# Kernel tuning notes

Measured on AMD Instinct MI355X. Metric: run time of the kernel, lower is better.

Reference implementation:

```python
import jax, jax.numpy as jnp
import numpy as np

B, L, D, H = 2, 2048, 1024, 16
DH = D // H  # per-head dim = 64


def setup_inputs() -> dict:
    key = jax.random.key(0)
    ks = jax.random.split(key, 7)
    s = 1.0 / np.sqrt(D)
    x = jax.random.normal(ks[0], (B, L, D), dtype=jnp.float32)
    Wq = jax.random.normal(ks[1], (D, D), dtype=jnp.float32) * s
    bq = jax.random.normal(ks[2], (D,), dtype=jnp.float32) * s
    Wk = jax.random.normal(ks[3], (D, D), dtype=jnp.float32) * s
    bk = jax.random.normal(ks[4], (D,), dtype=jnp.float32) * s
    Wv = jax.random.normal(ks[5], (D, D), dtype=jnp.float32) * s
    bv = jax.random.normal(ks[6], (D,), dtype=jnp.float32) * s
    # strict upper-triangular causal mask; mask==1 means position is masked (-inf)
    atten_mask = jnp.triu(jnp.ones((L, L), dtype=jnp.int32), k=1)
    return {"x": x, "atten_mask": atten_mask, "Wq": Wq, "bq": bq,
            "Wk": Wk, "bk": bk, "Wv": Wv, "bv": bv}


def reference(x, atten_mask, Wq, bq, Wk, bk, Wv, bv):
    # nn.Linear: y = x @ W^T + b
    q = x @ Wq.T + bq  # [B,L,D]
    k = x @ Wk.T + bk
    v = x @ Wv.T + bv
    # contiguous split into heads == reshape to [B,L,H,DH]
    q = q.reshape(B, L, H, DH)
    k = k.reshape(B, L, H, DH)
    v = v.reshape(B, L, H, DH)
    scale = jnp.sqrt(jnp.float32(DH))
    scores = jnp.einsum('blhd,bmhd->bhlm', q, k) / scale  # [B,H,L,L]
    # torch.where(mask == 1, -inf, scores)
    scores = jnp.where(atten_mask[None, None] == 1, -jnp.inf, scores)
    attn = jax.nn.softmax(scores, axis=-1)
    out = jnp.einsum('bhlm,bmhd->blhd', attn, v)  # [B,L,H,DH]
    return out.reshape(B, L, D)  # concat heads along channel dim
```

## Files before the change

### kernel.cpp

```cpp
#include <hip/hip_runtime.h>
#include <hip/hip_bf16.h>

#define BDIM 2
#define LSEQ 2048
#define DMODEL 1024
#define NH 16
#define DHEAD 64
#define SP 72
#define CTS 136

typedef __bf16 bf16_t;
typedef __attribute__((ext_vector_type(8))) __bf16 bf16x8;
typedef __attribute__((ext_vector_type(4))) __bf16 bf16x4;
typedef __attribute__((ext_vector_type(2))) __bf16 bf16x2;
typedef __attribute__((ext_vector_type(4))) float f32x4;
typedef __attribute__((ext_vector_type(4))) int i32x4;

static __device__ __forceinline__ f32x4 mfma16(bf16x8 a, bf16x8 b, f32x4 c) {
    return __builtin_amdgcn_mfma_f32_16x16x32_bf16(a, b, c, 0, 0, 0);
}

static __device__ __forceinline__ void load_lds16(const bf16_t* g, void* l) {
    __builtin_amdgcn_global_load_lds(
        (const __attribute__((address_space(1))) void*)g,
        (__attribute__((address_space(3))) void*)l, 16, 0, 0);
}

__global__ void convert_all(
    const float* __restrict__ x,
    const float* __restrict__ Wq, const float* __restrict__ Wk, const float* __restrict__ Wv,
    const float* __restrict__ bq, const float* __restrict__ bk, const float* __restrict__ bv,
    bf16_t* __restrict__ cx,
    bf16_t* __restrict__ cWq, bf16_t* __restrict__ cWk, bf16_t* __restrict__ cWv,
    bf16_t* __restrict__ cbq, bf16_t* __restrict__ cbk, bf16_t* __restrict__ cbv,
    float SQ)
{
    const int blk = blockIdx.x;
    const float* src; bf16_t* dst; int base, cnt; float sc = 1.0f;
    if (blk < 1024)      { src = x;  dst = cx;  base = blk * 1024;          cnt = 1024; }
    else if (blk < 1280) { src = Wq; dst = cWq; base = (blk - 1024) * 1024; cnt = 1024; sc = SQ; }
    else if (blk < 1536) { src = Wk; dst = cWk; base = (blk - 1280) * 1024; cnt = 1024; }
    else if (blk < 1792) { src = Wv; dst = cWv; base = (blk - 1536) * 1024; cnt = 1024; }
    else if (blk == 1792){ src = bq; dst = cbq; base = 0; cnt = 256; sc = SQ; }
    else if (blk == 1793){ src = bk; dst = cbk; base = 0; cnt = 256; }
    else                 { src = bv; dst = cbv; base = 0; cnt = 256; }

    for (int i = base + threadIdx.x; i < base + cnt; i += 256) {
        f32x4 v = *(const f32x4*)(src + 4 * (size_t)i);
        bf16x4 o;
        o[0] = (bf16_t)(v[0] * sc); o[1] = (bf16_t)(v[1] * sc);
        o[2] = (bf16_t)(v[2] * sc); o[3] = (bf16_t)(v[3] * sc);
        *(bf16x4*)(dst + 4 * (size_t)i) = o;
    }
}

__global__ __launch_bounds__(512, 2) void qkv_gemm(
    const bf16_t* __restrict__ x,
    const bf16_t* __restrict__ W0, const bf16_t* __restrict__ W1, const bf16_t* __restrict__ W2,
    const bf16_t* __restrict__ b0, const bf16_t* __restrict__ b1, const bf16_t* __restrict__ b2,
    bf16_t* __restrict__ yq, bf16_t* __restrict__ yk, bf16_t* __restrict__ yvT)
{
    __shared__ alignas(16) bf16_t smem[65536];

    const int tid  = threadIdx.x;
    const int lane = tid & 63;
    const int w    = tid >> 6;
    const int quad = lane >> 4;
    const int n16  = lane & 15;
    const int swz  = n16 & 7;
    const int srow = lane >> 3;
    const int schnk = (lane & 7) ^ srow;

    const int s   = blockIdx.x;
    const int sem = ((s & 7) << 3) | (s >> 3);
    const int m0  = (sem >> 2) * 256;
    const int n0  = (sem & 3) * 256;
    const int z   = blockIdx.y;

    const bf16_t* W    = (z == 0) ? W0 : ((z == 1) ? W1 : W2);
    const bf16_t* bias = (z == 0) ? b0 : ((z == 1) ? b1 : b2);

    const int wm = (w >> 2) * 128;
    const int wn = (w & 3) * 64;

    const bf16_t* gA = x + (size_t)(m0 + w * 8 + srow) * DMODEL + schnk * 8;
    const bf16_t* gB = W + (size_t)(n0 + w * 8 + srow) * DMODEL + schnk * 8;

    f32x4 acc[8][4] = {};

    auto stageA = [&](int buf, int h, int kt) {
        bf16_t* d = smem + buf * 32768 + (h * 128 + w * 8) * 64;
        const bf16_t* src = gA + (size_t)(h * 128) * DMODEL + kt * 64;
        load_lds16(src, d);
        load_lds16(src + (size_t)64 * DMODEL, d + 64 * 64);
    };
    auto stageB = [&](int buf, int h, int kt) {
        bf16_t* d = smem + buf * 32768 + 16384 + (h * 128 + w * 8) * 64;
        const bf16_t* src = gB + (size_t)(h * 128) * DMODEL + kt * 64;
        load_lds16(src, d);
        load_lds16(src + (size_t)64 * DMODEL, d + 64 * 64);
    };

    stageA(0, 0, 0); stageA(0, 1, 0);
    stageB(0, 0, 0); stageB(0, 1, 0);
    stageB(1, 0, 1); stageB(1, 1, 1);
    asm volatile("s_waitcnt vmcnt(4)" ::: "memory");
    __builtin_amdgcn_s_barrier();

    for (int u = 0; u < 16; ++u) {
        const int buf = u & 1;
        const bf16_t* Ab = smem + buf * 32768;
        const bf16_t* Bb = Ab + 16384;

        bf16x8 bfr[4][2], aX[2][2], aY[2][2];

        #pragma unroll
        for (int nt = 0; nt < 4; ++nt) {
            const bf16_t* br = Bb + (wn + nt * 16 + n16) * 64;
            bfr[nt][0] = *(const bf16x8*)(br + ((quad    ) ^ swz) * 8);
            bfr[nt][1] = *(const bf16x8*)(br + ((quad + 4) ^ swz) * 8);
        }
        #pragma unroll
        for (int m2 = 0; m2 < 2; ++m2) {
            const bf16_t* ar = Ab + (wm + m2 * 16 + n16) * 64;
            aX[m2][0] = *(const bf16x8*)(ar + ((quad    ) ^ swz) * 8);
            aX[m2][1] = *(const bf16x8*)(ar + ((quad + 4) ^ swz) * 8);
        }
        if (u + 1 < 16) { stageA(buf ^ 1, 0, u + 1); stageA(buf ^ 1, 1, u + 1); }
        asm volatile("s_waitcnt lgkmcnt(0)" ::: "memory");
        __builtin_amdgcn_s_barrier();
        if (u + 2 < 16) stageB(buf, 0, u + 2);

        #pragma unroll
        for (int m2 = 0; m2 < 2; ++m2) {
            const bf16_t* ar = Ab + (wm + (2 + m2) * 16 + n16) * 64;
            aY[m2][0] = *(const bf16x8*)(ar + ((quad    ) ^ swz) * 8);
            aY[m2][1] = *(const bf16x8*)(ar + ((quad + 4) ^ swz) * 8);
        }
        #pragma unroll
        for (int m2 = 0; m2 < 2; ++m2)
            #pragma unroll
            for (int nt = 0; nt < 4; ++nt) {
                acc[m2][nt] = mfma16(aX[m2][0], bfr[nt][0], acc[m2][nt]);
                acc[m2][nt] = mfma16(aX[m2][1], bfr[nt][1], acc[m2][nt]);
            }
        if (u + 2 < 16) stageB(buf, 1, u + 2);

        #pragma unroll
        for (int m2 = 0; m2 < 2; ++m2) {
            const bf16_t* ar = Ab + (wm + (4 + m2) * 16 + n16) * 64;
            aX[m2][0] = *(const bf16x8*)(ar + ((quad    ) ^ swz) * 8);
            aX[m2][1] = *(const bf16x8*)(ar + ((quad + 4) ^ swz) * 8);
        }
        #pragma unroll
        for (int m2 = 0; m2 < 2; ++m2)
            #pragma unroll
            for (int nt = 0; nt < 4; ++nt) {
                acc[2 + m2][nt] = mfma16(aY[m2][0], bfr[nt][0], acc[2 + m2][nt]);
                acc[2 + m2][nt] = mfma16(aY[m2][1], bfr[nt][1], acc[2 + m2][nt]);
            }

        #pragma unroll
        for (int m2 = 0; m2 < 2; ++m2) {
            const bf16_t* ar = Ab + (wm + (6 + m2) * 16 + n16) * 64;
            aY[m2][0] = *(const bf16x8*)(ar + ((quad    ) ^ swz) * 8);
            aY[m2][1] = *(const bf16x8*)(ar + ((quad + 4) ^ swz) * 8);
        }
        #pragma unroll
        for (int m2 = 0; m2 < 2; ++m2)
            #pragma unroll
            for (int nt = 0; nt < 4; ++nt) {
                acc[4 + m2][nt] = mfma16(aX[m2][0], bfr[nt][0], acc[4 + m2][nt]);
                acc[4 + m2][nt] = mfma16(aX[m2][1], bfr[nt][1], acc[4 + m2][nt]);
            }

        #pragma unroll
        for (int m2 = 0; m2 < 2; ++m2)
            #pragma unroll
            for (int nt = 0; nt < 4; ++nt) {
                acc[6 + m2][nt] = mfma16(aY[m2][0], bfr[nt][0], acc[6 + m2][nt]);
                acc[6 + m2][nt] = mfma16(aY[m2][1], bfr[nt][1], acc[6 + m2][nt]);
            }

        if (u < 14) asm volatile("s_waitcnt vmcnt(4)" ::: "memory");
        else        asm volatile("s_waitcnt vmcnt(0)" ::: "memory");
        __builtin_amdgcn_s_barrier();
    }

    if (z < 2) {
        bf16_t* y = (z == 0) ? yq : yk;
        bf16_t* Ct = smem;
        #pragma unroll
        for (int hp = 0; hp < 2; ++hp) {
            if (((w & 3) >> 1) == hp) {
                #pragma unroll
                for (int nt = 0; nt < 4; ++nt) {
                    const int jc = (w & 1) * 64 + nt * 16 + n16;
                    const float bv = (float)bias[n0 + hp * 128 + jc];
                    #pragma unroll
                    for (int mt = 0; mt < 8; ++mt) {
                        const int rr = wm + mt * 16 + quad * 4;
                        #pragma unroll
                        for (int r = 0; r < 4; ++r)
                            Ct[(rr + r) * CTS + jc] = (bf16_t)(acc[mt][nt][r] + bv);
                    }
                }
            }
            __syncthreads();
            const int row = tid >> 1;
            const int seg = tid & 1;
            const int hh  = (n0 >> 6) + hp * 2 + seg;
            const int i   = m0 + row;
            const int bb  = i >> 11, ll = i & 2047;
            bf16_t* dst = &y[(((size_t)bb * NH + hh) * LSEQ + ll) * DHEAD];
            const bf16_t* srcr = &Ct[row * CTS + seg * 64];
            #pragma unroll
            for (int c = 0; c < 8; ++c)
                *(bf16x8*)(dst + c * 8) = *(const bf16x8*)(srcr + c * 8);
            __syncthreads();
        }
    } else {
        #pragma unroll
        for (int nt = 0; nt < 4; ++nt) {
            const int j = n0 + wn + nt * 16 + n16;
            const float bv = (float)bias[j];
            #pragma unroll
            for (int mt = 0; mt < 8; ++mt) {
                const int i0 = m0 + wm + mt * 16 + quad * 4;
                const int bb = i0 >> 11, l = i0 & 2047;
                bf16x4 pk;
                #pragma unroll
                for (int r = 0; r < 4; ++r) pk[r] = (bf16_t)(acc[mt][nt][r] + bv);
                *(bf16x4*)(&yvT[((size_t)bb * DMODEL + j) * LSEQ + l]) = pk;
            }
        }
    }
}

__global__ __launch_bounds__(256) void attn_fused(
    const bf16_t* __restrict__ qp,
    const bf16_t* __restrict__ kp,
    const bf16_t* __restrict__ vtp,
    float* __restrict__ out,
    float* __restrict__ Opart,
    float* __restrict__ ml)
{
    __shared__ alignas(16) bf16_t Ks[2][64 * 64];
    __shared__ alignas(16) bf16_t Vs[2][64 * 64];
    __shared__ alignas(16) bf16_t Pw[4][2][32 * SP];

    const int tid  = threadIdx.x;
    const int lane = tid & 63;
    const int w    = tid >> 6;
    const int quad = lane >> 4;
    const int n16  = lane & 15;
    const int lane3 = lane >> 3;
    const int lane7 = lane & 7;
    const int swz8  = (lane7 ^ lane3) * 8;
    const int swz   = n16 & 7;

    const int bh  = blockIdx.x;
    const int yy  = blockIdx.y;
    const int p   = yy & 7;
    const bool isA = (yy < 8);
    const int b = bh >> 4, h = bh & 15;
    const size_t hb = (size_t)bh * (LSEQ * DHEAD);

    float l_[2];
    f32x4 oacc[2][4];

    auto process = [&](int qt, int t0, int ntiles, bool maskTail) {
        int iqg[2];
        bf16x8 qb[2][2];
        #pragma unroll
        for (int g = 0; g < 2; ++g) {
            iqg[g] = qt * 128 + 32 * w + 16 * g + n16;
            const bf16_t* qq = qp + hb + (size_t)iqg[g] * DHEAD;
            qb[g][0] = *(const bf16x8*)(qq + quad * 8);
            qb[g][1] = *(const bf16x8*)(qq + 32 + quad * 8);
        }

        const bf16_t* gk = kp  + hb + (size_t)(t0 * 64 + 16 * w + lane3) * DHEAD + swz8;
        const bf16_t* gv = vtp + hb + (size_t)(16 * w + lane3) * LSEQ + t0 * 64 + swz8;

        int buf = 0;
        {
            char* lk = (char*)&Ks[0][0] + w * 2048;
            char* lv = (char*)&Vs[0][0] + w * 2048;
            load_lds16(gk,             lk);
            load_lds16(gk + 8 * DHEAD, lk + 1024);
            load_lds16(gv,             lv);
            load_lds16(gv + 8 * LSEQ,  lv + 1024);
            gk += 64 * DHEAD; gv += 64;
        }
        __syncthreads();

        for (int it = 0; it < ntiles; ++it) {
            if (it + 1 < ntiles) {
                char* lk = (char*)&Ks[buf ^ 1][0] + w * 2048;
                char* lv = (char*)&Vs[buf ^ 1][0] + w * 2048;
                load_lds16(gk,             lk);
                load_lds16(gk + 8 * DHEAD, lk + 1024);
                load_lds16(gv,             lv);
                load_lds16(gv + 8 * LSEQ,  lv + 1024);
                gk += 64 * DHEAD; gv += 64;
            }

            const bf16_t* kb = &Ks[buf][0];
            f32x4 s[2][4];
            #pragma unroll
            for (int t = 0; t < 4; ++t) {
                const bf16_t* krow = kb + (t * 16 + n16) * 64;
                bf16x8 k0v = *(const bf16x8*)(krow + ((quad    ) ^ swz) * 8);
                bf16x8 k1v = *(const bf16x8*)(krow + ((quad + 4) ^ swz) * 8);
                #pragma unroll
                for (int g = 0; g < 2; ++g) {
                    f32x4 z = {0.f, 0.f, 0.f, 0.f};
                    z = mfma16(k0v, qb[g][0], z);
                    z = mfma16(k1v, qb[g][1], z);
                    s[g][t] = z;
                }
            }

            if (maskTail && it >= ntiles - 2) {
                const int k0 = (t0 + it) * 64;
                #pragma unroll
                for (int g = 0; g < 2; ++g)
                    #pragma unroll
                    for (int t = 0; t < 4; ++t)
                        #pragma unroll
                        for (int r = 0; r < 4; ++r)
                            if (k0 + t * 16 + quad * 4 + r > iqg[g]) s[g][t][r] = -1e30f;
            }

            #pragma unroll
            for (int g = 0; g < 2; ++g) {
                bf16_t* pw = &Pw[w][buf][g * 16 * SP] + n16 * SP + quad * 4;
                float rs = 0.f;
                #pragma unroll
                for (int t = 0; t < 4; ++t) {
                    float p0 = __builtin_amdgcn_exp2f(s[g][t][0]);
                    float p1 = __builtin_amdgcn_exp2f(s[g][t][1]);
                    float p2 = __builtin_amdgcn_exp2f(s[g][t][2]);
                    float p3 = __builtin_amdgcn_exp2f(s[g][t][3]);
                    rs += (p0 + p1) + (p2 + p3);
                    bf16x4 pk;
                    pk[0] = (bf16_t)p0; pk[1] = (bf16_t)p1;
                    pk[2] = (bf16_t)p2; pk[3] = (bf16_t)p3;
                    *(bf16x4*)(pw + t * 16) = pk;
                }
                l_[g] += rs;
            }

            asm volatile("s_waitcnt lgkmcnt(0)" ::: "memory");

            const bf16_t* vbs = &Vs[buf][0];
            #pragma unroll
            for (int c = 0; c < 2; ++c) {
                bf16x8 pb0 = *(const bf16x8*)(&Pw[w][buf][0]       + n16 * SP + c * 32 + quad * 8);
                bf16x8 pb1 = *(const bf16x8*)(&Pw[w][buf][16 * SP] + n16 * SP + c * 32 + quad * 8);
                #pragma unroll
                for (int t = 0; t < 4; ++t) {
                    const bf16_t* vrow = vbs + (t * 16 + n16) * 64;
                    bf16x8 va = *(const bf16x8*)(vrow + ((quad + 4 * c) ^ swz) * 8);
                    oacc[0][t] = mfma16(va, pb0, oacc[0][t]);
                    oacc[1][t] = mfma16(va, pb1, oacc[1][t]);
                }
            }

            __syncthreads();
            buf ^= 1;
        }
    };

    auto zero_state = [&]() {
        #pragma unroll
        for (int g = 0; g < 2; ++g) {
            l_[g] = 0.f;
            #pragma unroll
            for (int t = 0; t < 4; ++t) { f32x4 zz = {0.f,0.f,0.f,0.f}; oacc[g][t] = zz; }
        }
    };

    auto store_partial = [&](int pidx) {
        #pragma unroll
        for (int g = 0; g < 2; ++g) {
            float ls = l_[g];
            ls += __shfl_xor(ls, 16, 64);
            ls += __shfl_xor(ls, 32, 64);
            const int row = 32 * w + 16 * g + n16;
            float* Ob = Opart + (size_t)pidx * (128 * 64) + row * 64;
            #pragma unroll
            for (int t = 0; t < 4; ++t)
                *(f32x4*)(Ob + t * 16 + quad * 4) = oacc[g][t];
            if (quad == 0) ml[(size_t)pidx * 128 + row] = ls;
        }
    };

    if (isA) {
        zero_state();
        process(p, 0, 2 * p + 2, true);
        #pragma unroll
        for (int g = 0; g < 2; ++g) {
            float ls = l_[g];
            ls += __shfl_xor(ls, 16, 64);
            ls += __shfl_xor(ls, 32, 64);
            const float inv = 1.0f / ls;
            const int iq = p * 128 + 32 * w + 16 * g + n16;
            float* orow = out + ((size_t)b * LSEQ + iq) * DMODEL + h * DHEAD;
            #pragma unroll
            for (int t = 0; t < 4; ++t) {
                f32x4 o;
                o[0] = oacc[g][t][0] * inv; o[1] = oacc[g][t][1] * inv;
                o[2] = oacc[g][t][2] * inv; o[3] = oacc[g][t][3] * inv;
                *(f32x4*)(orow + t * 16 + quad * 4) = o;
            }
        }
        zero_state();
        process(15 - p, 0, 15 - 2 * p, false);
        store_partial((bh * 8 + (7 - p)) * 2 + 0);
    } else {
        zero_state();
        process(15 - p, 15 - 2 * p, 17, true);
        store_partial((bh * 8 + (7 - p)) * 2 + 1);
    }
}

__global__ __launch_bounds__(256) void attn_combine(
    const float* __restrict__ Opart, const float* __restrict__ ml,
    float* __restrict__ out)
{
    const int bh = blockIdx.x;
    const int q8 = blockIdx.y;
    const int t  = threadIdx.x;
    const int row = t >> 1;
    const int dh0 = (t & 1) * 32;
    const int p0  = (bh * 8 + q8) * 2;
    const int b = bh >> 4, h = bh & 15;

    float l0 = ml[(size_t)p0 * 128 + row];
    float l1 = ml[(size_t)(p0 + 1) * 128 + row];
    float inv = 1.0f / (l0 + l1);

    const float* P0 = Opart + (size_t)p0 * (128 * 64) + row * 64 + dh0;
    const float* P1 = P0 + 128 * 64;
    float* orow = out + ((size_t)b * LSEQ + ((8 + q8) * 128 + row)) * DMODEL
                + h * DHEAD + dh0;
    #pragma unroll
    for (int c = 0; c < 8; ++c) {
        f32x4 o0 = *(const f32x4*)(P0 + 4 * c);
        f32x4 o1 = *(const f32x4*)(P1 + 4 * c);
        f32x4 o;
        o[0] = (o0[0] + o1[0]) * inv;
        o[1] = (o0[1] + o1[1]) * inv;
        o[2] = (o0[2] + o1[2]) * inv;
        o[3] = (o0[3] + o1[3]) * inv;
        *(f32x4*)(orow + 4 * c) = o;
    }
}

extern "C" void kernel_launch(void* const* d_in, const int* in_sizes, int n_in,
                              void* d_out, int out_size, void* d_ws, size_t ws_size,
                              hipStream_t stream)
{
    const float* x  = (const float*)d_in[0];
    const float* Wq = (const float*)d_in[2];
    const float* bq = (const float*)d_in[3];
    const float* Wk = (const float*)d_in[4];
    const float* bk = (const float*)d_in[5];
    const float* Wv = (const float*)d_in[6];
    const float* bv = (const float*)d_in[7];
    float* out = (float*)d_out;

    char* ws = (char*)d_ws;
    bf16_t* q   = (bf16_t*)(ws);
    bf16_t* k   = (bf16_t*)(ws + 8u  * 1024 * 1024);
    bf16_t* vT  = (bf16_t*)(ws + 16u * 1024 * 1024);
    bf16_t* cx  = (bf16_t*)(ws + 24u * 1024 * 1024);
    bf16_t* cWq = (bf16_t*)(ws + 32u * 1024 * 1024);
    bf16_t* cWk = (bf16_t*)(ws + 34u * 1024 * 1024);
    bf16_t* cWv = (bf16_t*)(ws + 36u * 1024 * 1024);
    bf16_t* cbq = (bf16_t*)(ws + 38u * 1024 * 1024);
    bf16_t* cbk = (bf16_t*)(ws + 38u * 1024 * 1024 + 4096);
    bf16_t* cbv = (bf16_t*)(ws + 38u * 1024 * 1024 + 8192);
    float*  mlp = (float*) (ws + 39u * 1024 * 1024);
    float*  Op  = (float*) (ws + 40u * 1024 * 1024);

    const float SQ = 0.125f * 1.44269504088896f;

    convert_all<<<1795, 256, 0, stream>>>(x, Wq, Wk, Wv, bq, bk, bv,
                                          cx, cWq, cWk, cWv, cbq, cbk, cbv, SQ);

    dim3 g1(64, 3, 1);
    qkv_gemm<<<g1, 512, 0, stream>>>(cx, cWq, cWk, cWv, cbq, cbk, cbv, q, k, vT);

    dim3 g2(BDIM * NH, 16, 1);
    attn_fused<<<g2, 256, 0, stream>>>(q, k, vT, out, Op, mlp);

    dim3 g3(BDIM * NH, 8, 1);
    attn_combine<<<g3, 256, 0, stream>>>(Op, mlp, out);
}
```

Before: 171.1 us.

## Load V tiles straight into registers with double buffering instead of LDS

Drops the shared-memory V buffers in the fused attention kernel. Each wave now loads its V operand fragments directly from global memory into a pair of register arrays, prefetching the next tile while the current one is used, and the loop is unrolled by two to alternate buffers. A min-blocks hint of 2 is added to launch bounds, aiming for higher occupancy now that LDS use is smaller. In exchange, every wave reads the whole V tile on its own, so global/L2 traffic for V grows fourfold with short 64-byte row segments, and the extra register arrays raise VGPR pressure.

Result: slower. 179.2 us (+4.7%).

```diff
diff --git a/kernel.cpp b/kernel.cpp
--- a/kernel.cpp
+++ b/kernel.cpp
@@ -237,7 +237,7 @@
     }
 }
 
-__global__ __launch_bounds__(256) void attn_fused(
+__global__ __launch_bounds__(256, 2) void attn_fused(
     const bf16_t* __restrict__ qp,
     const bf16_t* __restrict__ kp,
     const bf16_t* __restrict__ vtp,
@@ -246,7 +246,6 @@
     float* __restrict__ ml)
 {
     __shared__ alignas(16) bf16_t Ks[2][64 * 64];
-    __shared__ alignas(16) bf16_t Vs[2][64 * 64];
     __shared__ alignas(16) bf16_t Pw[4][2][32 * SP];
 
     const int tid  = threadIdx.x;
@@ -280,30 +279,36 @@
             qb[g][1] = *(const bf16x8*)(qq + 32 + quad * 8);
         }
 
-        const bf16_t* gk = kp  + hb + (size_t)(t0 * 64 + 16 * w + lane3) * DHEAD + swz8;
-        const bf16_t* gv = vtp + hb + (size_t)(16 * w + lane3) * LSEQ + t0 * 64 + swz8;
+        const bf16_t* gk = kp + hb + (size_t)(t0 * 64 + 16 * w + lane3) * DHEAD + swz8;
+        const bf16_t* gvl = vtp + hb + (size_t)n16 * LSEQ + (size_t)t0 * 64 + quad * 8;
+
+        bf16x8 vA[8], vB[8];
+        auto loadV = [&](bf16x8 (&vv)[8], int it) {
+            const bf16_t* pv = gvl + it * 64;
+            #pragma unroll
+            for (int c = 0; c < 2; ++c)
+                #pragma unroll
+                for (int t = 0; t < 4; ++t)
+                    vv[c * 4 + t] = *(const bf16x8*)(pv + (size_t)(t * 16) * LSEQ + c * 32);
+        };
 
         int buf = 0;
         {
             char* lk = (char*)&Ks[0][0] + w * 2048;
-            char* lv = (char*)&Vs[0][0] + w * 2048;
             load_lds16(gk,             lk);
             load_lds16(gk + 8 * DHEAD, lk + 1024);
-            load_lds16(gv,             lv);
-            load_lds16(gv + 8 * LSEQ,  lv + 1024);
-            gk += 64 * DHEAD; gv += 64;
-        }
+            gk += 64 * DHEAD;
+        }
+        loadV(vA, 0);
         __syncthreads();
 
-        for (int it = 0; it < ntiles; ++it) {
+        auto body = [&](int it, bf16x8 (&vcur)[8], bf16x8 (&vnext)[8]) {
             if (it + 1 < ntiles) {
                 char* lk = (char*)&Ks[buf ^ 1][0] + w * 2048;
-                char* lv = (char*)&Vs[buf ^ 1][0] + w * 2048;
                 load_lds16(gk,             lk);
                 load_lds16(gk + 8 * DHEAD, lk + 1024);
-                load_lds16(gv,             lv);
-                load_lds16(gv + 8 * LSEQ,  lv + 1024);
-                gk += 64 * DHEAD; gv += 64;
+                gk += 64 * DHEAD;
+                loadV(vnext, it + 1);
             }
 
             const bf16_t* kb = &Ks[buf][0];
@@ -354,15 +359,13 @@
 
             asm volatile("s_waitcnt lgkmcnt(0)" ::: "memory");
 
-            const bf16_t* vbs = &Vs[buf][0];
             #pragma unroll
             for (int c = 0; c < 2; ++c) {
                 bf16x8 pb0 = *(const bf16x8*)(&Pw[w][buf][0]       + n16 * SP + c * 32 + quad * 8);
                 bf16x8 pb1 = *(const bf16x8*)(&Pw[w][buf][16 * SP] + n16 * SP + c * 32 + quad * 8);
                 #pragma unroll
                 for (int t = 0; t < 4; ++t) {
-                    const bf16_t* vrow = vbs + (t * 16 + n16) * 64;
-                    bf16x8 va = *(const bf16x8*)(vrow + ((quad + 4 * c) ^ swz) * 8);
+                    bf16x8 va = vcur[c * 4 + t];
                     oacc[0][t] = mfma16(va, pb0, oacc[0][t]);
                     oacc[1][t] = mfma16(va, pb1, oacc[1][t]);
                 }
@@ -370,7 +373,14 @@
 
             __syncthreads();
             buf ^= 1;
-        }
+        };
+
+        int it = 0;
+        for (; it + 2 <= ntiles; it += 2) {
+            body(it,     vA, vB);
+            body(it + 1, vB, vA);
+        }
+        if (it < ntiles) body(it, vA, vB);
     };
 
     auto zero_state = [&]() {
```

## Split attention waves 2x2 over query rows and key halves with LDS pair reduction

Applied to the files above, without the earlier changes.

Each pair of waves now covers 64 query rows, and each wave in the pair handles half of the 64 keys in every tile. This doubles reuse of each K/V LDS fragment per MFMA, and the two partial outputs and row sums are reduced through shared memory at the end. The LDS layout becomes a single 72KB arena that is shared with the reduction buffer, and launch bounds request two blocks per CU. The costs are higher register pressure (16 accumulator tiles per wave), a larger LDS footprint, and extra synchronisation in the reduction. Odd waves also sit idle during the epilogue.

Result: faster. 167.2 us (-2.3%).

```diff
diff --git a/kernel.cpp b/kernel.cpp
--- a/kernel.cpp
+++ b/kernel.cpp
@@ -6,7 +6,8 @@
 #define DMODEL 1024
 #define NH 16
 #define DHEAD 64
-#define SP 72
+#define SP 40
+#define RST 68
 #define CTS 136
 
 typedef __bf16 bf16_t;
@@ -237,7 +238,7 @@
     }
 }
 
-__global__ __launch_bounds__(256) void attn_fused(
+__global__ __launch_bounds__(256, 2) void attn_fused(
     const bf16_t* __restrict__ qp,
     const bf16_t* __restrict__ kp,
     const bf16_t* __restrict__ vtp,
@@ -245,9 +246,11 @@
     float* __restrict__ Opart,
     float* __restrict__ ml)
 {
-    __shared__ alignas(16) bf16_t Ks[2][64 * 64];
-    __shared__ alignas(16) bf16_t Vs[2][64 * 64];
-    __shared__ alignas(16) bf16_t Pw[4][2][32 * SP];
+    __shared__ alignas(16) char arena[73728];
+    bf16_t* KsB = (bf16_t*)(arena);
+    bf16_t* VsB = (bf16_t*)(arena + 16384);
+    bf16_t* PwB = (bf16_t*)(arena + 32768);
+    float*  Rex = (float*) (arena + 32768);
 
     const int tid  = threadIdx.x;
     const int lane = tid & 63;
@@ -259,6 +262,12 @@
     const int swz8  = (lane7 ^ lane3) * 8;
     const int swz   = n16 & 7;
 
+    const int wq   = (w >> 1) * 64;
+    const int wkv  = (w & 1) * 32;
+    const int pairI = w >> 1;
+    const bool isOdd = (w & 1) != 0;
+    bf16_t* Pw0 = PwB + w * (2 * 64 * SP);
+
     const int bh  = blockIdx.x;
     const int yy  = blockIdx.y;
     const int p   = yy & 7;
@@ -266,15 +275,24 @@
     const int b = bh >> 4, h = bh & 15;
     const size_t hb = (size_t)bh * (LSEQ * DHEAD);
 
-    float l_[2];
-    f32x4 oacc[2][4];
+    float l_[4];
+    f32x4 oacc[4][4];
+
+    auto zero_state = [&]() {
+        #pragma unroll
+        for (int g = 0; g < 4; ++g) {
+            l_[g] = 0.f;
+            #pragma unroll
+            for (int mv = 0; mv < 4; ++mv) { f32x4 zz = {0.f,0.f,0.f,0.f}; oacc[mv][g] = zz; }
+        }
+    };
 
     auto process = [&](int qt, int t0, int ntiles, bool maskTail) {
-        int iqg[2];
-        bf16x8 qb[2][2];
-        #pragma unroll
-        for (int g = 0; g < 2; ++g) {
-            iqg[g] = qt * 128 + 32 * w + 16 * g + n16;
+        int iqg[4];
+        bf16x8 qb[4][2];
+        #pragma unroll
+        for (int g = 0; g < 4; ++g) {
+            iqg[g] = qt * 128 + wq + 16 * g + n16;
             const bf16_t* qq = qp + hb + (size_t)iqg[g] * DHEAD;
             qb[g][0] = *(const bf16x8*)(qq + quad * 8);
             qb[g][1] = *(const bf16x8*)(qq + 32 + quad * 8);
@@ -285,8 +303,8 @@
 
         int buf = 0;
         {
-            char* lk = (char*)&Ks[0][0] + w * 2048;
-            char* lv = (char*)&Vs[0][0] + w * 2048;
+            char* lk = (char*)KsB + w * 2048;
+            char* lv = (char*)VsB + w * 2048;
             load_lds16(gk,             lk);
             load_lds16(gk + 8 * DHEAD, lk + 1024);
             load_lds16(gv,             lv);
@@ -297,8 +315,8 @@
 
         for (int it = 0; it < ntiles; ++it) {
             if (it + 1 < ntiles) {
-                char* lk = (char*)&Ks[buf ^ 1][0] + w * 2048;
-                char* lv = (char*)&Vs[buf ^ 1][0] + w * 2048;
+                char* lk = (char*)KsB + (buf ^ 1) * 8192 + w * 2048;
+                char* lv = (char*)VsB + (buf ^ 1) * 8192 + w * 2048;
                 load_lds16(gk,             lk);
                 load_lds16(gk + 8 * DHEAD, lk + 1024);
                 load_lds16(gv,             lv);
@@ -306,66 +324,66 @@
                 gk += 64 * DHEAD; gv += 64;
             }
 
-            const bf16_t* kb = &Ks[buf][0];
+            const bf16_t* kb = KsB + buf * 4096;
             f32x4 s[2][4];
             #pragma unroll
-            for (int t = 0; t < 4; ++t) {
-                const bf16_t* krow = kb + (t * 16 + n16) * 64;
+            for (int m = 0; m < 2; ++m) {
+                const bf16_t* krow = kb + (wkv + 16 * m + n16) * 64;
                 bf16x8 k0v = *(const bf16x8*)(krow + ((quad    ) ^ swz) * 8);
                 bf16x8 k1v = *(const bf16x8*)(krow + ((quad + 4) ^ swz) * 8);
                 #pragma unroll
-                for (int g = 0; g < 2; ++g) {
+                for (int g = 0; g < 4; ++g) {
                     f32x4 z = {0.f, 0.f, 0.f, 0.f};
                     z = mfma16(k0v, qb[g][0], z);
                     z = mfma16(k1v, qb[g][1], z);
-                    s[g][t] = z;
+                    s[m][g] = z;
                 }
             }
 
             if (maskTail && it >= ntiles - 2) {
-                const int k0 = (t0 + it) * 64;
-                #pragma unroll
-                for (int g = 0; g < 2; ++g)
+                const int k0 = (t0 + it) * 64 + wkv;
+                #pragma unroll
+                for (int m = 0; m < 2; ++m)
                     #pragma unroll
-                    for (int t = 0; t < 4; ++t)
+                    for (int g = 0; g < 4; ++g)
                         #pragma unroll
                         for (int r = 0; r < 4; ++r)
-                            if (k0 + t * 16 + quad * 4 + r > iqg[g]) s[g][t][r] = -1e30f;
-            }
-
-            #pragma unroll
-            for (int g = 0; g < 2; ++g) {
-                bf16_t* pw = &Pw[w][buf][g * 16 * SP] + n16 * SP + quad * 4;
+                            if (k0 + 16 * m + quad * 4 + r > iqg[g]) s[m][g][r] = -1e30f;
+            }
+
+            bf16_t* pwb = Pw0 + buf * (64 * SP);
+            #pragma unroll
+            for (int g = 0; g < 4; ++g) {
                 float rs = 0.f;
                 #pragma unroll
-                for (int t = 0; t < 4; ++t) {
-                    float p0 = __builtin_amdgcn_exp2f(s[g][t][0]);
-                    float p1 = __builtin_amdgcn_exp2f(s[g][t][1]);
-                    float p2 = __builtin_amdgcn_exp2f(s[g][t][2]);
-                    float p3 = __builtin_amdgcn_exp2f(s[g][t][3]);
+                for (int m = 0; m < 2; ++m) {
+                    float p0 = __builtin_amdgcn_exp2f(s[m][g][0]);
+                    float p1 = __builtin_amdgcn_exp2f(s[m][g][1]);
+                    float p2 = __builtin_amdgcn_exp2f(s[m][g][2]);
+                    float p3 = __builtin_amdgcn_exp2f(s[m][g][3]);
                     rs += (p0 + p1) + (p2 + p3);
                     bf16x4 pk;
                     pk[0] = (bf16_t)p0; pk[1] = (bf16_t)p1;
                     pk[2] = (bf16_t)p2; pk[3] = (bf16_t)p3;
-                    *(bf16x4*)(pw + t * 16) = pk;
+                    *(bf16x4*)(pwb + (16 * g + n16) * SP + 16 * m + quad * 4) = pk;
                 }
                 l_[g] += rs;
             }
 
             asm volatile("s_waitcnt lgkmcnt(0)" ::: "memory");
 
-            const bf16_t* vbs = &Vs[buf][0];
-            #pragma unroll
-            for (int c = 0; c < 2; ++c) {
-                bf16x8 pb0 = *(const bf16x8*)(&Pw[w][buf][0]       + n16 * SP + c * 32 + quad * 8);
-                bf16x8 pb1 = *(const bf16x8*)(&Pw[w][buf][16 * SP] + n16 * SP + c * 32 + quad * 8);
-                #pragma unroll
-                for (int t = 0; t < 4; ++t) {
-                    const bf16_t* vrow = vbs + (t * 16 + n16) * 64;
-                    bf16x8 va = *(const bf16x8*)(vrow + ((quad + 4 * c) ^ swz) * 8);
-                    oacc[0][t] = mfma16(va, pb0, oacc[0][t]);
-                    oacc[1][t] = mfma16(va, pb1, oacc[1][t]);
-                }
+            const bf16_t* vb = VsB + buf * 4096;
+            bf16x8 pb[4];
+            #pragma unroll
+            for (int g = 0; g < 4; ++g)
+                pb[g] = *(const bf16x8*)(pwb + (16 * g + n16) * SP + quad * 8);
+            #pragma unroll
+            for (int mv = 0; mv < 4; ++mv) {
+                const bf16_t* vrow = vb + (16 * mv + n16) * 64;
+                bf16x8 va = *(const bf16x8*)(vrow + ((((w & 1) * 4) + quad) ^ swz) * 8);
+                #pragma unroll
+                for (int g = 0; g < 4; ++g)
+                    oacc[mv][g] = mfma16(va, pb[g], oacc[mv][g]);
             }
 
             __syncthreads();
@@ -373,55 +391,76 @@
         }
     };
 
-    auto zero_state = [&]() {
-        #pragma unroll
-        for (int g = 0; g < 2; ++g) {
-            l_[g] = 0.f;
-            #pragma unroll
-            for (int t = 0; t < 4; ++t) { f32x4 zz = {0.f,0.f,0.f,0.f}; oacc[g][t] = zz; }
+    auto reduce_pair = [&]() {
+        __syncthreads();
+        float* Rb = Rex + pairI * (64 * RST);
+        if (isOdd) {
+            #pragma unroll
+            for (int g = 0; g < 4; ++g) {
+                #pragma unroll
+                for (int mv = 0; mv < 4; ++mv)
+                    *(f32x4*)(Rb + (16 * g + n16) * RST + 16 * mv + quad * 4) = oacc[mv][g];
+                Rb[(16 * g + n16) * RST + 64 + quad] = l_[g];
+            }
+        }
+        __syncthreads();
+        if (!isOdd) {
+            #pragma unroll
+            for (int g = 0; g < 4; ++g) {
+                #pragma unroll
+                for (int mv = 0; mv < 4; ++mv) {
+                    f32x4 t = *(const f32x4*)(Rb + (16 * g + n16) * RST + 16 * mv + quad * 4);
+                    oacc[mv][g][0] += t[0]; oacc[mv][g][1] += t[1];
+                    oacc[mv][g][2] += t[2]; oacc[mv][g][3] += t[3];
+                }
+                float ls = l_[g] + Rb[(16 * g + n16) * RST + 64 + quad];
+                ls += __shfl_xor(ls, 16, 64);
+                ls += __shfl_xor(ls, 32, 64);
+                l_[g] = ls;
+            }
         }
     };
 
     auto store_partial = [&](int pidx) {
-        #pragma unroll
-        for (int g = 0; g < 2; ++g) {
-            float ls = l_[g];
-            ls += __shfl_xor(ls, 16, 64);
-            ls += __shfl_xor(ls, 32, 64);
-            const int row = 32 * w + 16 * g + n16;
+        if (isOdd) return;
+        #pragma unroll
+        for (int g = 0; g < 4; ++g) {
+            const int row = wq + 16 * g + n16;
             float* Ob = Opart + (size_t)pidx * (128 * 64) + row * 64;
             #pragma unroll
-            for (int t = 0; t < 4; ++t)
-                *(f32x4*)(Ob + t * 16 + quad * 4) = oacc[g][t];
-            if (quad == 0) ml[(size_t)pidx * 128 + row] = ls;
+            for (int mv = 0; mv < 4; ++mv)
+                *(f32x4*)(Ob + 16 * mv + quad * 4) = oacc[mv][g];
+            if (quad == 0) ml[(size_t)pidx * 128 + row] = l_[g];
         }
     };
 
     if (isA) {
         zero_state();
         process(p, 0, 2 * p + 2, true);
-        #pragma unroll
-        for (int g = 0; g < 2; ++g) {
-            float ls = l_[g];
-            ls += __shfl_xor(ls, 16, 64);
-            ls += __shfl_xor(ls, 32, 64);
-            const float inv = 1.0f / ls;
-            const int iq = p * 128 + 32 * w + 16 * g + n16;
-            float* orow = out + ((size_t)b * LSEQ + iq) * DMODEL + h * DHEAD;
-            #pragma unroll
-            for (int t = 0; t < 4; ++t) {
-                f32x4 o;
-                o[0] = oacc[g][t][0] * inv; o[1] = oacc[g][t][1] * inv;
-                o[2] = oacc[g][t][2] * inv; o[3] = oacc[g][t][3] * inv;
-                *(f32x4*)(orow + t * 16 + quad * 4) = o;
+        reduce_pair();
+        if (!isOdd) {
+            #pragma unroll
+            for (int g = 0; g < 4; ++g) {
+                const float inv = 1.0f / l_[g];
+                const int iq = p * 128 + wq + 16 * g + n16;
+                float* orow = out + ((size_t)b * LSEQ + iq) * DMODEL + h * DHEAD;
+                #pragma unroll
+                for (int mv = 0; mv < 4; ++mv) {
+                    f32x4 o;
+                    o[0] = oacc[mv][g][0] * inv; o[1] = oacc[mv][g][1] * inv;
+                    o[2] = oacc[mv][g][2] * inv; o[3] = oacc[mv][g][3] * inv;
+                    *(f32x4*)(orow + 16 * mv + quad * 4) = o;
+                }
             }
         }
         zero_state();
         process(15 - p, 0, 15 - 2 * p, false);
+        reduce_pair();
         store_partial((bh * 8 + (7 - p)) * 2 + 0);
     } else {
         zero_state();
         process(15 - p, 15 - 2 * p, 17, true);
+        reduce_pair();
         store_partial((bh * 8 + (7 - p)) * 2 + 1);
     }
 }
```
